# Performance work log

Measured on AMD Instinct MI355X. Metric: run time of the kernel, lower is better.

## Reference

```python
import jax, jax.numpy as jnp
import numpy as np

N, D, K = 40000, 64, 16
E = N * K
EPS = 1e-5  # torch BatchNorm1d default eps


def _bn(h, g, b):
    # BatchNorm1d in training mode: biased batch statistics over dim 0
    m = h.mean(0)
    v = h.var(0)
    return (h - m) * jax.lax.rsqrt(v + EPS) * g + b


def setup_inputs() -> dict:
    key = jax.random.key(0)
    ks = jax.random.split(key, 4)
    kp = jax.random.split(ks[3], 9)

    def w(k, shape):
        return (jax.random.normal(k, shape, dtype=jnp.float32) / np.float32(np.sqrt(shape[0])))

    src = jax.random.randint(ks[2], (E,), 0, N, dtype=jnp.int32)
    dst = jnp.repeat(jnp.arange(N, dtype=jnp.int32), K)  # kNN-style: each node has K in-edges

    return {
        "x": jax.random.normal(ks[0], (N, D), dtype=jnp.float32),
        "pos": jax.random.normal(ks[1], (N, 3), dtype=jnp.float32),
        "edge_index": jnp.stack([src, dst]),
        "W_in": w(kp[0], (D, D)),
        "g1": jnp.ones(D), "b1": jnp.zeros(D),
        "W_v": w(kp[1], (D, D)),
        "W_src": w(kp[2], (D, D)),
        "W_dst": w(kp[3], (D, D)),
        "Wp1": w(kp[4], (3, 3)), "bp1": jnp.zeros(3),
        "gp": jnp.ones(3), "bp": jnp.zeros(3),
        "Wp2": w(kp[5], (3, D)), "bp2": jnp.zeros(D),
        "ga0": jnp.ones(D), "ba0": jnp.zeros(D),
        "Wa1": w(kp[6], (D, D // 8)), "ba1": jnp.zeros(D // 8),
        "ga1": jnp.ones(D // 8), "bb1": jnp.zeros(D // 8),
        "Wa2": w(kp[7], (D // 8, D)), "ba2": jnp.zeros(D),
        "g2": jnp.ones(D), "b2": jnp.zeros(D),
        "W_out": w(kp[8], (D, D)),
        "g3": jnp.ones(D), "b3": jnp.zeros(D),
    }


def reference(x, pos, edge_index, W_in, g1, b1, W_v, W_src, W_dst,
              Wp1, bp1, gp, bp, Wp2, bp2, ga0, ba0, Wa1, ba1, ga1, bb1,
              Wa2, ba2, g2, b2, W_out, g3, b3):
    src, dst = edge_index[0], edge_index[1]  # j (source), i (dest)
    n = x.shape[0]
    x_skip = x
    h = jax.nn.relu(_bn(x @ W_in, g1, b1))

    # PointTransformerConv
    a_src = h @ W_src            # alpha_j projection [N,D]
    a_dst = h @ W_dst            # alpha_i projection [N,D]
    v = h @ W_v                  # value projection  [N,D]
    rel = pos[dst] - pos[src]    # pos_i - pos_j     [E,3]
    ph = jax.nn.relu(_bn(rel @ Wp1 + bp1, gp, bp))
    delta = ph @ Wp2 + bp2       # pos_nn output     [E,D]
    a = a_dst[dst] - a_src[src] + delta
    # attn_nn: BN -> ReLU -> (Lin+BN+ReLU) -> Lin
    a = jax.nn.relu(_bn(a, ga0, ba0))
    a = jax.nn.relu(_bn(a @ Wa1 + ba1, ga1, bb1))
    a = a @ Wa2 + ba2            # [E,D]
    # segment-wise softmax over incoming edges of each dest node
    amax = jax.lax.stop_gradient(jax.ops.segment_max(a, dst, num_segments=n))
    e = jnp.exp(a - amax[dst])
    s = jax.ops.segment_sum(e, dst, num_segments=n)
    attn = e / (s[dst] + 1e-16)  # PyG softmax adds 1e-16
    agg = jax.ops.segment_sum(attn * (v[src] + delta), dst, num_segments=n)

    h = jax.nn.relu(_bn(agg, g2, b2))
    h = _bn(h @ W_out, g3, b3)
    return jax.nn.relu(h + x_skip)
```

## Files before the change

### kernel.cpp

```cpp
#include <hip/hip_runtime.h>

#define NN 40000
#define DDIM 64
#define KE 16
#define EE 640000
#define BNEPS 1e-5f

#define WAVE_FENCE() asm volatile("" ::: "memory")

__device__ __forceinline__ void bn_coeff(const float* __restrict__ S, int C, int c,
                                         const float* __restrict__ g, const float* __restrict__ b,
                                         float inv_n, float& sc, float& sh)
{
    float m   = S[c] * inv_n;
    float var = S[C + c] * inv_n - m * m;
    float r   = rsqrtf(var + BNEPS);
    sc = g[c] * r;
    sh = b[c] - m * sc;
}

template<int TRN>
__global__ __launch_bounds__(256) void gemm64_k(
    const float* __restrict__ in,
    const float* __restrict__ W0, const float* __restrict__ W1, const float* __restrict__ W2,
    float* __restrict__ out0, float* __restrict__ out1, float* __restrict__ out2,
    const float* __restrict__ Sin, const float* __restrict__ gamma, const float* __restrict__ beta,
    float inv_n, float* __restrict__ Sout)
{
    const float* W = (blockIdx.y == 0) ? W0 : ((blockIdx.y == 1) ? W1 : W2);
    float* out     = (blockIdx.y == 0) ? out0 : ((blockIdx.y == 1) ? out1 : out2);

    __shared__ float Wl[64][64];
    __shared__ float inl[64][65];
    __shared__ float scl[64], shl[64];
    __shared__ float ssum[64], ssq[64];

    const int t = threadIdx.x;
    if (t < 64) {
        if (TRN) { float sc, sh; bn_coeff(Sin, 64, t, gamma, beta, inv_n, sc, sh); scl[t] = sc; shl[t] = sh; }
        ssum[t] = 0.f; ssq[t] = 0.f;
    }
#pragma unroll
    for (int i = 0; i < 16; i++) { int idx = t + i * 256; Wl[idx >> 6][idx & 63] = W[idx]; }
    __syncthreads();

    const int rbase = blockIdx.x * 64;
    {
        const int d = t & 63;
        float sc = 0.f, sh = 0.f;
        if (TRN) { sc = scl[d]; sh = shl[d]; }
#pragma unroll
        for (int i = 0; i < 16; i++) {
            int r = (t >> 6) + i * 4;
            float v = in[(size_t)(rbase + r) * 64 + d];
            if (TRN) v = fmaxf(fmaf(v, sc, sh), 0.f);
            inl[r][d] = v;
        }
    }
    __syncthreads();

    const int c0 = (t & 15) * 4, r0 = (t >> 4) * 4;
    float acc[4][4] = {};
#pragma unroll 16
    for (int d = 0; d < 64; d++) {
        float4 w4 = *(const float4*)&Wl[d][c0];
#pragma unroll
        for (int i = 0; i < 4; i++) {
            float h = inl[r0 + i][d];
            acc[i][0] = fmaf(h, w4.x, acc[i][0]);
            acc[i][1] = fmaf(h, w4.y, acc[i][1]);
            acc[i][2] = fmaf(h, w4.z, acc[i][2]);
            acc[i][3] = fmaf(h, w4.w, acc[i][3]);
        }
    }
#pragma unroll
    for (int i = 0; i < 4; i++) {
        float4 o; o.x = acc[i][0]; o.y = acc[i][1]; o.z = acc[i][2]; o.w = acc[i][3];
        *(float4*)&out[(size_t)(rbase + r0 + i) * 64 + c0] = o;
    }
    if (Sout) {
#pragma unroll
        for (int j = 0; j < 4; j++) {
            float s  = acc[0][j] + acc[1][j] + acc[2][j] + acc[3][j];
            float qv = acc[0][j] * acc[0][j] + acc[1][j] * acc[1][j] + acc[2][j] * acc[2][j] + acc[3][j] * acc[3][j];
            atomicAdd(&ssum[c0 + j], s);
            atomicAdd(&ssq[c0 + j], qv);
        }
        __syncthreads();
        if (t < 64) { atomicAdd(&Sout[t], ssum[t]); atomicAdd(&Sout[64 + t], ssq[t]); }
    }
}

__global__ __launch_bounds__(256) void edge_q_k(
    const float* __restrict__ pos, const int* __restrict__ src,
    const float* __restrict__ Wp1, const float* __restrict__ bp1,
    float4* __restrict__ q4, float* __restrict__ Sq)
{
    float w00 = Wp1[0], w01 = Wp1[1], w02 = Wp1[2];
    float w10 = Wp1[3], w11 = Wp1[4], w12 = Wp1[5];
    float w20 = Wp1[6], w21 = Wp1[7], w22 = Wp1[8];
    float c0 = bp1[0], c1 = bp1[1], c2 = bp1[2];
    float s0 = 0, s1 = 0, s2 = 0, p0 = 0, p1 = 0, p2 = 0;
    for (int e = blockIdx.x * blockDim.x + threadIdx.x; e < EE; e += gridDim.x * blockDim.x) {
        int sj = src[e]; int di = e >> 4;
        float r0 = pos[di * 3 + 0] - pos[sj * 3 + 0];
        float r1 = pos[di * 3 + 1] - pos[sj * 3 + 1];
        float r2 = pos[di * 3 + 2] - pos[sj * 3 + 2];
        float v0 = c0 + r0 * w00 + r1 * w10 + r2 * w20;
        float v1 = c1 + r0 * w01 + r1 * w11 + r2 * w21;
        float v2 = c2 + r0 * w02 + r1 * w12 + r2 * w22;
        float4 o; o.x = v0; o.y = v1; o.z = v2; o.w = __int_as_float(sj);
        q4[e] = o;
        s0 += v0; s1 += v1; s2 += v2;
        p0 += v0 * v0; p1 += v1 * v1; p2 += v2 * v2;
    }
#pragma unroll
    for (int o = 32; o > 0; o >>= 1) {
        s0 += __shfl_down(s0, o); s1 += __shfl_down(s1, o); s2 += __shfl_down(s2, o);
        p0 += __shfl_down(p0, o); p1 += __shfl_down(p1, o); p2 += __shfl_down(p2, o);
    }
    __shared__ float sred[4][6];
    const int w = threadIdx.x >> 6;
    if ((threadIdx.x & 63) == 0) {
        sred[w][0] = s0; sred[w][1] = s1; sred[w][2] = s2;
        sred[w][3] = p0; sred[w][4] = p1; sred[w][5] = p2;
    }
    __syncthreads();
    if (threadIdx.x < 6) {
        float v = sred[0][threadIdx.x] + sred[1][threadIdx.x] + sred[2][threadIdx.x] + sred[3][threadIdx.x];
        atomicAdd(&Sq[threadIdx.x], v);
    }
}

__global__ __launch_bounds__(256) void edge_a0_k(
    const float4* __restrict__ q4v,
    const float* __restrict__ adst, const float* __restrict__ asrc,
    const float* __restrict__ Wp2, const float* __restrict__ bp2,
    const float* __restrict__ Sq, const float* __restrict__ gp, const float* __restrict__ bp_,
    float* __restrict__ Sa0)
{
    const int lane = threadIdx.x & 63;
    const int r = lane >> 4, fq = lane & 15;
    const int wv   = blockIdx.x * (blockDim.x >> 6) + (threadIdx.x >> 6);
    const int nwv  = gridDim.x * (blockDim.x >> 6);
    const float inv_e = 1.0f / (float)EE;
    float sc30, sh30, sc31, sh31, sc32, sh32;
    bn_coeff(Sq, 3, 0, gp, bp_, inv_e, sc30, sh30);
    bn_coeff(Sq, 3, 1, gp, bp_, inv_e, sc31, sh31);
    bn_coeff(Sq, 3, 2, gp, bp_, inv_e, sc32, sh32);
    float4 w0_4 = *(const float4*)&Wp2[fq * 4];
    float4 w1_4 = *(const float4*)&Wp2[64 + fq * 4];
    float4 w2_4 = *(const float4*)&Wp2[128 + fq * 4];
    float4 bd4  = *(const float4*)&bp2[fq * 4];
    float4 s4 = {0.f,0.f,0.f,0.f}, p4 = {0.f,0.f,0.f,0.f};

    for (int i = wv; i < NN; i += nwv) {
        const int e0 = i << 4;
        float4 ad4 = *(const float4*)&adst[(size_t)i * 64 + fq * 4];
        float4 qs  = q4v[e0 + (lane & 15)];
        int sv = __float_as_int(qs.w);
        int sj[4];
#pragma unroll
        for (int p = 0; p < 4; p++) sj[p] = __shfl(sv, p * 4 + r);
        float4 av[4];
#pragma unroll
        for (int p = 0; p < 4; p++) av[p] = *(const float4*)&asrc[(size_t)sj[p] * 64 + fq * 4];
#pragma unroll
        for (int p = 0; p < 4; p++) {
            int j = p * 4 + r;
            float ph0 = fmaxf(fmaf(__shfl(qs.x, j), sc30, sh30), 0.f);
            float ph1 = fmaxf(fmaf(__shfl(qs.y, j), sc31, sh31), 0.f);
            float ph2 = fmaxf(fmaf(__shfl(qs.z, j), sc32, sh32), 0.f);
            float4 a0v;
            a0v.x = ad4.x - av[p].x + bd4.x + ph0 * w0_4.x + ph1 * w1_4.x + ph2 * w2_4.x;
            a0v.y = ad4.y - av[p].y + bd4.y + ph0 * w0_4.y + ph1 * w1_4.y + ph2 * w2_4.y;
            a0v.z = ad4.z - av[p].z + bd4.z + ph0 * w0_4.z + ph1 * w1_4.z + ph2 * w2_4.z;
            a0v.w = ad4.w - av[p].w + bd4.w + ph0 * w0_4.w + ph1 * w1_4.w + ph2 * w2_4.w;
            s4.x += a0v.x; s4.y += a0v.y; s4.z += a0v.z; s4.w += a0v.w;
            p4.x = fmaf(a0v.x, a0v.x, p4.x); p4.y = fmaf(a0v.y, a0v.y, p4.y);
            p4.z = fmaf(a0v.z, a0v.z, p4.z); p4.w = fmaf(a0v.w, a0v.w, p4.w);
        }
    }
    s4.x += __shfl_xor(s4.x, 16); s4.y += __shfl_xor(s4.y, 16);
    s4.z += __shfl_xor(s4.z, 16); s4.w += __shfl_xor(s4.w, 16);
    p4.x += __shfl_xor(p4.x, 16); p4.y += __shfl_xor(p4.y, 16);
    p4.z += __shfl_xor(p4.z, 16); p4.w += __shfl_xor(p4.w, 16);
    s4.x += __shfl_xor(s4.x, 32); s4.y += __shfl_xor(s4.y, 32);
    s4.z += __shfl_xor(s4.z, 32); s4.w += __shfl_xor(s4.w, 32);
    p4.x += __shfl_xor(p4.x, 32); p4.y += __shfl_xor(p4.y, 32);
    p4.z += __shfl_xor(p4.z, 32); p4.w += __shfl_xor(p4.w, 32);

    __shared__ float ls[64], lq[64];
    if (threadIdx.x < 64) { ls[threadIdx.x] = 0.f; lq[threadIdx.x] = 0.f; }
    __syncthreads();
    if (lane < 16) {
        atomicAdd(&ls[fq * 4 + 0], s4.x); atomicAdd(&ls[fq * 4 + 1], s4.y);
        atomicAdd(&ls[fq * 4 + 2], s4.z); atomicAdd(&ls[fq * 4 + 3], s4.w);
        atomicAdd(&lq[fq * 4 + 0], p4.x); atomicAdd(&lq[fq * 4 + 1], p4.y);
        atomicAdd(&lq[fq * 4 + 2], p4.z); atomicAdd(&lq[fq * 4 + 3], p4.w);
    }
    __syncthreads();
    if (threadIdx.x < 64) { atomicAdd(&Sa0[threadIdx.x], ls[threadIdx.x]); atomicAdd(&Sa0[64 + threadIdx.x], lq[threadIdx.x]); }
}

__global__ __launch_bounds__(256) void edge_t_k(
    const float4* __restrict__ q4v,
    const float* __restrict__ adst, const float* __restrict__ asrc,
    const float* __restrict__ Wp2, const float* __restrict__ bp2,
    const float* __restrict__ Sq, const float* __restrict__ gp, const float* __restrict__ bp_,
    const float* __restrict__ Sa0, const float* __restrict__ ga0, const float* __restrict__ ba0,
    const float* __restrict__ Wa1, const float* __restrict__ ba1,
    float* __restrict__ tout, float* __restrict__ St)
{
    __shared__ float a1l[64][68];
    __shared__ float wl[64][8];
    __shared__ float red[16];
    const int t = threadIdx.x, lane = t & 63, w = t >> 6;
    const int r = lane >> 4, fq = lane & 15;
    const float inv_e = 1.0f / (float)EE;
    float sc30, sh30, sc31, sh31, sc32, sh32;
    bn_coeff(Sq, 3, 0, gp, bp_, inv_e, sc30, sh30);
    bn_coeff(Sq, 3, 1, gp, bp_, inv_e, sc31, sh31);
    bn_coeff(Sq, 3, 2, gp, bp_, inv_e, sc32, sh32);
    float4 scA4, shA4;
    bn_coeff(Sa0, 64, fq * 4 + 0, ga0, ba0, inv_e, scA4.x, shA4.x);
    bn_coeff(Sa0, 64, fq * 4 + 1, ga0, ba0, inv_e, scA4.y, shA4.y);
    bn_coeff(Sa0, 64, fq * 4 + 2, ga0, ba0, inv_e, scA4.z, shA4.z);
    bn_coeff(Sa0, 64, fq * 4 + 3, ga0, ba0, inv_e, scA4.w, shA4.w);
    float4 w0_4 = *(const float4*)&Wp2[fq * 4];
    float4 w1_4 = *(const float4*)&Wp2[64 + fq * 4];
    float4 w2_4 = *(const float4*)&Wp2[128 + fq * 4];
    float4 bd4  = *(const float4*)&bp2[fq * 4];
    for (int i = t; i < 512; i += 256) wl[i >> 3][i & 7] = Wa1[i];
    if (t < 16) red[t] = 0.f;
    __syncthreads();

    const int eLl = lane >> 2;
    const int j0  = (lane & 3) * 2;
    float bA = ba1[j0], bB = ba1[j0 + 1];
    float ssA = 0.f, spA = 0.f, ssB = 0.f, spB = 0.f;

    for (int i = blockIdx.x * 4 + w; i < NN; i += gridDim.x * 4) {
        const int e0 = i << 4;
        {
            float4 ad4 = *(const float4*)&adst[(size_t)i * 64 + fq * 4];
            float4 qs  = q4v[e0 + (lane & 15)];
            int sv = __float_as_int(qs.w);
            int sj[4];
#pragma unroll
            for (int p = 0; p < 4; p++) sj[p] = __shfl(sv, p * 4 + r);
            float4 av[4];
#pragma unroll
            for (int p = 0; p < 4; p++) av[p] = *(const float4*)&asrc[(size_t)sj[p] * 64 + fq * 4];
#pragma unroll
            for (int p = 0; p < 4; p++) {
                int j = p * 4 + r;
                float ph0 = fmaxf(fmaf(__shfl(qs.x, j), sc30, sh30), 0.f);
                float ph1 = fmaxf(fmaf(__shfl(qs.y, j), sc31, sh31), 0.f);
                float ph2 = fmaxf(fmaf(__shfl(qs.z, j), sc32, sh32), 0.f);
                float4 a1v;
                a1v.x = ad4.x - av[p].x + bd4.x + ph0 * w0_4.x + ph1 * w1_4.x + ph2 * w2_4.x;
                a1v.y = ad4.y - av[p].y + bd4.y + ph0 * w0_4.y + ph1 * w1_4.y + ph2 * w2_4.y;
                a1v.z = ad4.z - av[p].z + bd4.z + ph0 * w0_4.z + ph1 * w1_4.z + ph2 * w2_4.z;
                a1v.w = ad4.w - av[p].w + bd4.w + ph0 * w0_4.w + ph1 * w1_4.w + ph2 * w2_4.w;
                a1v.x = fmaxf(fmaf(a1v.x, scA4.x, shA4.x), 0.f);
                a1v.y = fmaxf(fmaf(a1v.y, scA4.y, shA4.y), 0.f);
                a1v.z = fmaxf(fmaf(a1v.z, scA4.z, shA4.z), 0.f);
                a1v.w = fmaxf(fmaf(a1v.w, scA4.w, shA4.w), 0.f);
                *(float4*)&a1l[w * 16 + j][fq * 4] = a1v;
            }
        }
        WAVE_FENCE();
        {
            float acc0 = bA, acc1 = bB;
#pragma unroll 16
            for (int dd = 0; dd < 64; dd++) {
                float a = a1l[w * 16 + eLl][dd];
                acc0 = fmaf(a, wl[dd][j0], acc0);
                acc1 = fmaf(a, wl[dd][j0 + 1], acc1);
            }
            int e = e0 + eLl;
            float2 o; o.x = acc0; o.y = acc1;
            *(float2*)&tout[(size_t)e * 8 + j0] = o;
            ssA += acc0; spA += acc0 * acc0;
            ssB += acc1; spB += acc1 * acc1;
        }
        WAVE_FENCE();
    }
    __syncthreads();
    atomicAdd(&red[j0], ssA);     atomicAdd(&red[j0 + 1], ssB);
    atomicAdd(&red[8 + j0], spA); atomicAdd(&red[8 + j0 + 1], spB);
    __syncthreads();
    if (t < 16) atomicAdd(&St[t], red[t]);
}

__global__ __launch_bounds__(256) void edge_final_k(
    const float* __restrict__ tin,
    const float4* __restrict__ q4v, const float* __restrict__ vv,
    const float* __restrict__ Wp2, const float* __restrict__ bp2,
    const float* __restrict__ Sq, const float* __restrict__ gp, const float* __restrict__ bp_,
    const float* __restrict__ St, const float* __restrict__ ga1, const float* __restrict__ bb1,
    const float* __restrict__ Wa2, const float* __restrict__ ba2,
    float* __restrict__ agg, float* __restrict__ Sagg)
{
    __shared__ float att_l[4][16][68];
    __shared__ float tt_l[4][16][8];
    __shared__ float ls[64], lq[64];
    const int t = threadIdx.x, lane = t & 63, w = t >> 6;
    const int r = lane >> 4, fq = lane & 15;
    const float inv_e = 1.0f / (float)EE;
    float sc3[3], sh3[3];
#pragma unroll
    for (int k = 0; k < 3; k++) bn_coeff(Sq, 3, k, gp, bp_, inv_e, sc3[k], sh3[k]);
    float sc8[8], sh8[8];
#pragma unroll
    for (int k = 0; k < 8; k++) bn_coeff(St, 8, k, ga1, bb1, inv_e, sc8[k], sh8[k]);
    float wa[8];
#pragma unroll
    for (int k = 0; k < 8; k++) wa[k] = Wa2[k * 64 + lane];
    float bad = ba2[lane];
    float4 wp0_4 = *(const float4*)&Wp2[fq * 4];
    float4 wp1_4 = *(const float4*)&Wp2[64 + fq * 4];
    float4 wp2_4 = *(const float4*)&Wp2[128 + fq * 4];
    float4 bpd4  = *(const float4*)&bp2[fq * 4];
    float4 ssum4 = {0.f, 0.f, 0.f, 0.f}, ssq4 = {0.f, 0.f, 0.f, 0.f};

    for (int nn = 0; nn < 4; nn++) {
        const int i  = blockIdx.x * 16 + nn * 4 + w;
        const int e0 = i << 4;
        if (lane < 32) {
            float4 v = *(const float4*)&tin[(size_t)e0 * 8 + lane * 4];
            ((float4*)&tt_l[w][0][0])[lane] = v;
        }
        float4 qs = q4v[e0 + (lane & 15)];
        int sv = __float_as_int(qs.w);
        WAVE_FENCE();
        {
            float ax[16];
            float m = -3.0e38f;
#pragma unroll
            for (int j = 0; j < 16; j++) {
                float4 ta = *(const float4*)&tt_l[w][j][0];
                float4 tb = *(const float4*)&tt_l[w][j][4];
                float a = bad;
                a = fmaf(fmaxf(fmaf(ta.x, sc8[0], sh8[0]), 0.f), wa[0], a);
                a = fmaf(fmaxf(fmaf(ta.y, sc8[1], sh8[1]), 0.f), wa[1], a);
                a = fmaf(fmaxf(fmaf(ta.z, sc8[2], sh8[2]), 0.f), wa[2], a);
                a = fmaf(fmaxf(fmaf(ta.w, sc8[3], sh8[3]), 0.f), wa[3], a);
                a = fmaf(fmaxf(fmaf(tb.x, sc8[4], sh8[4]), 0.f), wa[4], a);
                a = fmaf(fmaxf(fmaf(tb.y, sc8[5], sh8[5]), 0.f), wa[5], a);
                a = fmaf(fmaxf(fmaf(tb.z, sc8[6], sh8[6]), 0.f), wa[6], a);
                a = fmaf(fmaxf(fmaf(tb.w, sc8[7], sh8[7]), 0.f), wa[7], a);
                ax[j] = a; m = fmaxf(m, a);
            }
            float s = 0.f;
#pragma unroll
            for (int j = 0; j < 16; j++) { ax[j] = __expf(ax[j] - m); s += ax[j]; }
            float inv = 1.0f / (s + 1e-16f);
#pragma unroll
            for (int j = 0; j < 16; j++) att_l[w][j][lane] = ax[j] * inv;
        }
        WAVE_FENCE();
        {
            float4 acc = {0.f, 0.f, 0.f, 0.f};
#pragma unroll
            for (int p = 0; p < 4; p++) {
                int j  = p * 4 + r;
                int sj = __shfl(sv, j);
                float4 v4  = *(const float4*)&vv[(size_t)sj * 64 + fq * 4];
                float4 at4 = *(const float4*)&att_l[w][j][fq * 4];
                float ph0 = fmaxf(fmaf(__shfl(qs.x, j), sc3[0], sh3[0]), 0.f);
                float ph1 = fmaxf(fmaf(__shfl(qs.y, j), sc3[1], sh3[1]), 0.f);
                float ph2 = fmaxf(fmaf(__shfl(qs.z, j), sc3[2], sh3[2]), 0.f);
                float4 dl4;
                dl4.x = bpd4.x + ph0 * wp0_4.x + ph1 * wp1_4.x + ph2 * wp2_4.x;
                dl4.y = bpd4.y + ph0 * wp0_4.y + ph1 * wp1_4.y + ph2 * wp2_4.y;
                dl4.z = bpd4.z + ph0 * wp0_4.z + ph1 * wp1_4.z + ph2 * wp2_4.z;
                dl4.w = bpd4.w + ph0 * wp0_4.w + ph1 * wp1_4.w + ph2 * wp2_4.w;
                acc.x = fmaf(at4.x, v4.x + dl4.x, acc.x);
                acc.y = fmaf(at4.y, v4.y + dl4.y, acc.y);
                acc.z = fmaf(at4.z, v4.z + dl4.z, acc.z);
                acc.w = fmaf(at4.w, v4.w + dl4.w, acc.w);
            }
            acc.x += __shfl_xor(acc.x, 16); acc.y += __shfl_xor(acc.y, 16);
            acc.z += __shfl_xor(acc.z, 16); acc.w += __shfl_xor(acc.w, 16);
            acc.x += __shfl_xor(acc.x, 32); acc.y += __shfl_xor(acc.y, 32);
            acc.z += __shfl_xor(acc.z, 32); acc.w += __shfl_xor(acc.w, 32);
            if (lane < 16) {
                *(float4*)&agg[(size_t)i * 64 + lane * 4] = acc;
                ssum4.x += acc.x; ssum4.y += acc.y; ssum4.z += acc.z; ssum4.w += acc.w;
                ssq4.x  += acc.x * acc.x; ssq4.y += acc.y * acc.y;
                ssq4.z  += acc.z * acc.z; ssq4.w += acc.w * acc.w;
            }
        }
        WAVE_FENCE();
    }
    if (t < 64) { ls[t] = 0.f; lq[t] = 0.f; }
    __syncthreads();
    if (lane < 16) {
        atomicAdd(&ls[fq * 4 + 0], ssum4.x); atomicAdd(&ls[fq * 4 + 1], ssum4.y);
        atomicAdd(&ls[fq * 4 + 2], ssum4.z); atomicAdd(&ls[fq * 4 + 3], ssum4.w);
        atomicAdd(&lq[fq * 4 + 0], ssq4.x);  atomicAdd(&lq[fq * 4 + 1], ssq4.y);
        atomicAdd(&lq[fq * 4 + 2], ssq4.z);  atomicAdd(&lq[fq * 4 + 3], ssq4.w);
    }
    __syncthreads();
    if (t < 64) { atomicAdd(&Sagg[t], ls[t]); atomicAdd(&Sagg[64 + t], lq[t]); }
}

__global__ __launch_bounds__(256) void final_k(
    const float* __restrict__ t2, const float* __restrict__ x,
    const float* __restrict__ St2, const float* __restrict__ g3, const float* __restrict__ b3,
    float* __restrict__ out)
{
    __shared__ float scl[64], shl[64];
    const int t = threadIdx.x;
    if (t < 64) { float sc, sh; bn_coeff(St2, 64, t, g3, b3, 1.0f / (float)NN, sc, sh); scl[t] = sc; shl[t] = sh; }
    __syncthreads();
    int idx = blockIdx.x * 256 + t;
    int c0 = (idx & 15) * 4;
    const float4 a = *(const float4*)&t2[(size_t)idx * 4];
    const float4 b = *(const float4*)&x[(size_t)idx * 4];
    float4 o;
    o.x = fmaxf(fmaf(a.x, scl[c0 + 0], shl[c0 + 0]) + b.x, 0.f);
    o.y = fmaxf(fmaf(a.y, scl[c0 + 1], shl[c0 + 1]) + b.y, 0.f);
    o.z = fmaxf(fmaf(a.z, scl[c0 + 2], shl[c0 + 2]) + b.z, 0.f);
    o.w = fmaxf(fmaf(a.w, scl[c0 + 3], shl[c0 + 3]) + b.w, 0.f);
    *(float4*)&out[(size_t)idx * 4] = o;
}

extern "C" void kernel_launch(void* const* d_in, const int* in_sizes, int n_in,
                              void* d_out, int out_size, void* d_ws, size_t ws_size,
                              hipStream_t stream)
{
    const float* x    = (const float*)d_in[0];
    const float* pos  = (const float*)d_in[1];
    const int*   src  = (const int*)d_in[2];
    const float* W_in = (const float*)d_in[3];
    const float* g1   = (const float*)d_in[4];
    const float* b1   = (const float*)d_in[5];
    const float* W_v  = (const float*)d_in[6];
    const float* W_src= (const float*)d_in[7];
    const float* W_dst= (const float*)d_in[8];
    const float* Wp1  = (const float*)d_in[9];
    const float* bp1  = (const float*)d_in[10];
    const float* gp   = (const float*)d_in[11];
    const float* bp_  = (const float*)d_in[12];
    const float* Wp2  = (const float*)d_in[13];
    const float* bp2  = (const float*)d_in[14];
    const float* ga0  = (const float*)d_in[15];
    const float* ba0  = (const float*)d_in[16];
    const float* Wa1  = (const float*)d_in[17];
    const float* ba1  = (const float*)d_in[18];
    const float* ga1  = (const float*)d_in[19];
    const float* bb1  = (const float*)d_in[20];
    const float* Wa2  = (const float*)d_in[21];
    const float* ba2  = (const float*)d_in[22];
    const float* g2   = (const float*)d_in[23];
    const float* b2   = (const float*)d_in[24];
    const float* W_out= (const float*)d_in[25];
    const float* g3   = (const float*)d_in[26];
    const float* b3   = (const float*)d_in[27];
    float* out = (float*)d_out;

    float* wsf   = (float*)d_ws;
    float* S_t1  = wsf;
    float* S_q   = wsf + 128;
    float* S_a0  = wsf + 192;
    float* S_t   = wsf + 320;
    float* S_agg = wsf + 384;
    float* S_t2  = wsf + 512;
    const size_t N64 = (size_t)NN * 64;
    float* t1   = wsf + 1024;
    float* asrc = t1 + N64;
    float* adst = asrc + N64;
    float* vv   = adst + N64;
    float* q4   = vv + N64;
    float* tt   = q4 + 4 * (size_t)EE;
    float* agg  = t1;
    float* t2   = asrc;

    hipMemsetAsync(wsf, 0, 1024 * sizeof(float), stream);

    gemm64_k<0><<<dim3(625, 1), 256, 0, stream>>>(x, W_in, W_in, W_in, t1, t1, t1,
                                                  nullptr, nullptr, nullptr, 0.f, S_t1);
    gemm64_k<1><<<dim3(625, 3), 256, 0, stream>>>(t1, W_src, W_dst, W_v, asrc, adst, vv,
                                                  S_t1, g1, b1, 1.0f / (float)NN, nullptr);
    edge_q_k<<<256, 256, 0, stream>>>(pos, src, Wp1, bp1, (float4*)q4, S_q);
    edge_a0_k<<<2048, 256, 0, stream>>>((const float4*)q4, adst, asrc, Wp2, bp2, S_q, gp, bp_, S_a0);
    edge_t_k<<<2048, 256, 0, stream>>>((const float4*)q4, adst, asrc, Wp2, bp2, S_q, gp, bp_,
                                       S_a0, ga0, ba0, Wa1, ba1, tt, S_t);
    edge_final_k<<<2500, 256, 0, stream>>>(tt, (const float4*)q4, vv, Wp2, bp2, S_q, gp, bp_,
                                           S_t, ga1, bb1, Wa2, ba2, agg, S_agg);
    gemm64_k<1><<<dim3(625, 1), 256, 0, stream>>>(agg, W_out, W_out, W_out, t2, t2, t2,
                                                  S_agg, g2, b2, 1.0f / (float)NN, S_t2);
    final_k<<<2500, 256, 0, stream>>>(t2, x, S_t2, g3, b3, out);
}
```

Measured before the change: 290.9 us.

## Merge edge position kernel into first GEMM launch and reuse input tile across three projections

The independent edge position-encoding pass is folded into the first GEMM launch as extra blocks, so the two run concurrently and one launch is removed. The three-projection GEMM now loads and normalizes each input tile once and loops over the three weight matrices, rather than using three separate y-blocks that each reload the input. This cuts launch overhead and redundant input reads and BN application, at the cost of fewer blocks and serialized weight loads within each block for the projection GEMM.

```diff
diff --git a/kernel.cpp b/kernel.cpp
--- a/kernel.cpp
+++ b/kernel.cpp
@@ -19,46 +19,182 @@
     sh = b[c] - m * sc;
 }
 
-template<int TRN>
-__global__ __launch_bounds__(256) void gemm64_k(
+__global__ __launch_bounds__(256) void gemm0q_k(
+    const float* __restrict__ in, const float* __restrict__ W,
+    float* __restrict__ out, float* __restrict__ Sout,
+    const float* __restrict__ pos, const int* __restrict__ src,
+    const float* __restrict__ Wp1, const float* __restrict__ bp1,
+    float4* __restrict__ q4, float* __restrict__ Sq)
+{
+    const int t = threadIdx.x;
+    if (blockIdx.x < 625) {
+        __shared__ float Wl[64][64];
+        __shared__ float inl[64][65];
+        __shared__ float ssum[64], ssq[64];
+        if (t < 64) { ssum[t] = 0.f; ssq[t] = 0.f; }
+#pragma unroll
+        for (int i = 0; i < 16; i++) { int idx = t + i * 256; Wl[idx >> 6][idx & 63] = W[idx]; }
+        const int rbase = blockIdx.x * 64;
+        {
+            const int d = t & 63;
+#pragma unroll
+            for (int i = 0; i < 16; i++) {
+                int r = (t >> 6) + i * 4;
+                inl[r][d] = in[(size_t)(rbase + r) * 64 + d];
+            }
+        }
+        __syncthreads();
+        const int c0 = (t & 15) * 4, r0 = (t >> 4) * 4;
+        float acc[4][4] = {};
+#pragma unroll 16
+        for (int d = 0; d < 64; d++) {
+            float4 w4 = *(const float4*)&Wl[d][c0];
+#pragma unroll
+            for (int i = 0; i < 4; i++) {
+                float h = inl[r0 + i][d];
+                acc[i][0] = fmaf(h, w4.x, acc[i][0]);
+                acc[i][1] = fmaf(h, w4.y, acc[i][1]);
+                acc[i][2] = fmaf(h, w4.z, acc[i][2]);
+                acc[i][3] = fmaf(h, w4.w, acc[i][3]);
+            }
+        }
+#pragma unroll
+        for (int i = 0; i < 4; i++) {
+            float4 o; o.x = acc[i][0]; o.y = acc[i][1]; o.z = acc[i][2]; o.w = acc[i][3];
+            *(float4*)&out[(size_t)(rbase + r0 + i) * 64 + c0] = o;
+        }
+#pragma unroll
+        for (int j = 0; j < 4; j++) {
+            float s  = acc[0][j] + acc[1][j] + acc[2][j] + acc[3][j];
+            float qv = acc[0][j] * acc[0][j] + acc[1][j] * acc[1][j] + acc[2][j] * acc[2][j] + acc[3][j] * acc[3][j];
+            atomicAdd(&ssum[c0 + j], s);
+            atomicAdd(&ssq[c0 + j], qv);
+        }
+        __syncthreads();
+        if (t < 64) { atomicAdd(&Sout[t], ssum[t]); atomicAdd(&Sout[64 + t], ssq[t]); }
+    } else {
+        __shared__ float sred[4][6];
+        const int bq = blockIdx.x - 625;
+        float w00 = Wp1[0], w01 = Wp1[1], w02 = Wp1[2];
+        float w10 = Wp1[3], w11 = Wp1[4], w12 = Wp1[5];
+        float w20 = Wp1[6], w21 = Wp1[7], w22 = Wp1[8];
+        float c0 = bp1[0], c1 = bp1[1], c2 = bp1[2];
+        float s0 = 0, s1 = 0, s2 = 0, p0 = 0, p1 = 0, p2 = 0;
+        for (int e = bq * 256 + t; e < EE; e += 160 * 256) {
+            int sj = src[e]; int di = e >> 4;
+            float r0 = pos[di * 3 + 0] - pos[sj * 3 + 0];
+            float r1 = pos[di * 3 + 1] - pos[sj * 3 + 1];
+            float r2 = pos[di * 3 + 2] - pos[sj * 3 + 2];
+            float v0 = c0 + r0 * w00 + r1 * w10 + r2 * w20;
+            float v1 = c1 + r0 * w01 + r1 * w11 + r2 * w21;
+            float v2 = c2 + r0 * w02 + r1 * w12 + r2 * w22;
+            float4 o; o.x = v0; o.y = v1; o.z = v2; o.w = __int_as_float(sj);
+            q4[e] = o;
+            s0 += v0; s1 += v1; s2 += v2;
+            p0 += v0 * v0; p1 += v1 * v1; p2 += v2 * v2;
+        }
+#pragma unroll
+        for (int o = 32; o > 0; o >>= 1) {
+            s0 += __shfl_down(s0, o); s1 += __shfl_down(s1, o); s2 += __shfl_down(s2, o);
+            p0 += __shfl_down(p0, o); p1 += __shfl_down(p1, o); p2 += __shfl_down(p2, o);
+        }
+        const int w = t >> 6;
+        if ((t & 63) == 0) {
+            sred[w][0] = s0; sred[w][1] = s1; sred[w][2] = s2;
+            sred[w][3] = p0; sred[w][4] = p1; sred[w][5] = p2;
+        }
+        __syncthreads();
+        if (t < 6) {
+            float v = sred[0][t] + sred[1][t] + sred[2][t] + sred[3][t];
+            atomicAdd(&Sq[t], v);
+        }
+    }
+}
+
+__global__ __launch_bounds__(256) void gemm3_k(
     const float* __restrict__ in,
     const float* __restrict__ W0, const float* __restrict__ W1, const float* __restrict__ W2,
     float* __restrict__ out0, float* __restrict__ out1, float* __restrict__ out2,
     const float* __restrict__ Sin, const float* __restrict__ gamma, const float* __restrict__ beta,
+    float inv_n)
+{
+    __shared__ float Wl[64][64];
+    __shared__ float inl[64][65];
+    __shared__ float scl[64], shl[64];
+    const int t = threadIdx.x;
+    if (t < 64) { float sc, sh; bn_coeff(Sin, 64, t, gamma, beta, inv_n, sc, sh); scl[t] = sc; shl[t] = sh; }
+    __syncthreads();
+    const int rbase = blockIdx.x * 64;
+    {
+        const int d = t & 63;
+        float sc = scl[d], sh = shl[d];
+#pragma unroll
+        for (int i = 0; i < 16; i++) {
+            int r = (t >> 6) + i * 4;
+            float v = in[(size_t)(rbase + r) * 64 + d];
+            inl[r][d] = fmaxf(fmaf(v, sc, sh), 0.f);
+        }
+    }
+    const int c0 = (t & 15) * 4, r0 = (t >> 4) * 4;
+#pragma unroll
+    for (int ph = 0; ph < 3; ph++) {
+        const float* W = (ph == 0) ? W0 : ((ph == 1) ? W1 : W2);
+        float* out     = (ph == 0) ? out0 : ((ph == 1) ? out1 : out2);
+        __syncthreads();
+#pragma unroll
+        for (int i = 0; i < 16; i++) { int idx = t + i * 256; Wl[idx >> 6][idx & 63] = W[idx]; }
+        __syncthreads();
+        float acc[4][4] = {};
+#pragma unroll 16
+        for (int d = 0; d < 64; d++) {
+            float4 w4 = *(const float4*)&Wl[d][c0];
+#pragma unroll
+            for (int i = 0; i < 4; i++) {
+                float h = inl[r0 + i][d];
+                acc[i][0] = fmaf(h, w4.x, acc[i][0]);
+                acc[i][1] = fmaf(h, w4.y, acc[i][1]);
+                acc[i][2] = fmaf(h, w4.z, acc[i][2]);
+                acc[i][3] = fmaf(h, w4.w, acc[i][3]);
+            }
+        }
+#pragma unroll
+        for (int i = 0; i < 4; i++) {
+            float4 o; o.x = acc[i][0]; o.y = acc[i][1]; o.z = acc[i][2]; o.w = acc[i][3];
+            *(float4*)&out[(size_t)(rbase + r0 + i) * 64 + c0] = o;
+        }
+    }
+}
+
+__global__ __launch_bounds__(256) void gemm1_k(
+    const float* __restrict__ in, const float* __restrict__ W,
+    float* __restrict__ out,
+    const float* __restrict__ Sin, const float* __restrict__ gamma, const float* __restrict__ beta,
     float inv_n, float* __restrict__ Sout)
 {
-    const float* W = (blockIdx.y == 0) ? W0 : ((blockIdx.y == 1) ? W1 : W2);
-    float* out     = (blockIdx.y == 0) ? out0 : ((blockIdx.y == 1) ? out1 : out2);
-
     __shared__ float Wl[64][64];
     __shared__ float inl[64][65];
     __shared__ float scl[64], shl[64];
     __shared__ float ssum[64], ssq[64];
-
     const int t = threadIdx.x;
     if (t < 64) {
-        if (TRN) { float sc, sh; bn_coeff(Sin, 64, t, gamma, beta, inv_n, sc, sh); scl[t] = sc; shl[t] = sh; }
+        float sc, sh; bn_coeff(Sin, 64, t, gamma, beta, inv_n, sc, sh); scl[t] = sc; shl[t] = sh;
         ssum[t] = 0.f; ssq[t] = 0.f;
     }
 #pragma unroll
     for (int i = 0; i < 16; i++) { int idx = t + i * 256; Wl[idx >> 6][idx & 63] = W[idx]; }
     __syncthreads();
-
     const int rbase = blockIdx.x * 64;
     {
         const int d = t & 63;
-        float sc = 0.f, sh = 0.f;
-        if (TRN) { sc = scl[d]; sh = shl[d]; }
+        float sc = scl[d], sh = shl[d];
 #pragma unroll
         for (int i = 0; i < 16; i++) {
             int r = (t >> 6) + i * 4;
             float v = in[(size_t)(rbase + r) * 64 + d];
-            if (TRN) v = fmaxf(fmaf(v, sc, sh), 0.f);
-            inl[r][d] = v;
-        }
-    }
-    __syncthreads();
-
+            inl[r][d] = fmaxf(fmaf(v, sc, sh), 0.f);
+        }
+    }
+    __syncthreads();
     const int c0 = (t & 15) * 4, r0 = (t >> 4) * 4;
     float acc[4][4] = {};
 #pragma unroll 16
@@ -78,58 +214,15 @@
         float4 o; o.x = acc[i][0]; o.y = acc[i][1]; o.z = acc[i][2]; o.w = acc[i][3];
         *(float4*)&out[(size_t)(rbase + r0 + i) * 64 + c0] = o;
     }
-    if (Sout) {
-#pragma unroll
-        for (int j = 0; j < 4; j++) {
-            float s  = acc[0][j] + acc[1][j] + acc[2][j] + acc[3][j];
-            float qv = acc[0][j] * acc[0][j] + acc[1][j] * acc[1][j] + acc[2][j] * acc[2][j] + acc[3][j] * acc[3][j];
-            atomicAdd(&ssum[c0 + j], s);
-            atomicAdd(&ssq[c0 + j], qv);
-        }
-        __syncthreads();
-        if (t < 64) { atomicAdd(&Sout[t], ssum[t]); atomicAdd(&Sout[64 + t], ssq[t]); }
-    }
-}
-
-__global__ __launch_bounds__(256) void edge_q_k(
-    const float* __restrict__ pos, const int* __restrict__ src,
-    const float* __restrict__ Wp1, const float* __restrict__ bp1,
-    float4* __restrict__ q4, float* __restrict__ Sq)
-{
-    float w00 = Wp1[0], w01 = Wp1[1], w02 = Wp1[2];
-    float w10 = Wp1[3], w11 = Wp1[4], w12 = Wp1[5];
-    float w20 = Wp1[6], w21 = Wp1[7], w22 = Wp1[8];
-    float c0 = bp1[0], c1 = bp1[1], c2 = bp1[2];
-    float s0 = 0, s1 = 0, s2 = 0, p0 = 0, p1 = 0, p2 = 0;
-    for (int e = blockIdx.x * blockDim.x + threadIdx.x; e < EE; e += gridDim.x * blockDim.x) {
-        int sj = src[e]; int di = e >> 4;
-        float r0 = pos[di * 3 + 0] - pos[sj * 3 + 0];
-        float r1 = pos[di * 3 + 1] - pos[sj * 3 + 1];
-        float r2 = pos[di * 3 + 2] - pos[sj * 3 + 2];
-        float v0 = c0 + r0 * w00 + r1 * w10 + r2 * w20;
-        float v1 = c1 + r0 * w01 + r1 * w11 + r2 * w21;
-        float v2 = c2 + r0 * w02 + r1 * w12 + r2 * w22;
-        float4 o; o.x = v0; o.y = v1; o.z = v2; o.w = __int_as_float(sj);
-        q4[e] = o;
-        s0 += v0; s1 += v1; s2 += v2;
-        p0 += v0 * v0; p1 += v1 * v1; p2 += v2 * v2;
-    }
-#pragma unroll
-    for (int o = 32; o > 0; o >>= 1) {
-        s0 += __shfl_down(s0, o); s1 += __shfl_down(s1, o); s2 += __shfl_down(s2, o);
-        p0 += __shfl_down(p0, o); p1 += __shfl_down(p1, o); p2 += __shfl_down(p2, o);
-    }
-    __shared__ float sred[4][6];
-    const int w = threadIdx.x >> 6;
-    if ((threadIdx.x & 63) == 0) {
-        sred[w][0] = s0; sred[w][1] = s1; sred[w][2] = s2;
-        sred[w][3] = p0; sred[w][4] = p1; sred[w][5] = p2;
-    }
-    __syncthreads();
-    if (threadIdx.x < 6) {
-        float v = sred[0][threadIdx.x] + sred[1][threadIdx.x] + sred[2][threadIdx.x] + sred[3][threadIdx.x];
-        atomicAdd(&Sq[threadIdx.x], v);
-    }
+#pragma unroll
+    for (int j = 0; j < 4; j++) {
+        float s  = acc[0][j] + acc[1][j] + acc[2][j] + acc[3][j];
+        float qv = acc[0][j] * acc[0][j] + acc[1][j] * acc[1][j] + acc[2][j] * acc[2][j] + acc[3][j] * acc[3][j];
+        atomicAdd(&ssum[c0 + j], s);
+        atomicAdd(&ssq[c0 + j], qv);
+    }
+    __syncthreads();
+    if (t < 64) { atomicAdd(&Sout[t], ssum[t]); atomicAdd(&Sout[64 + t], ssq[t]); }
 }
 
 __global__ __launch_bounds__(256) void edge_a0_k(
@@ -481,17 +574,14 @@
 
     hipMemsetAsync(wsf, 0, 1024 * sizeof(float), stream);
 
-    gemm64_k<0><<<dim3(625, 1), 256, 0, stream>>>(x, W_in, W_in, W_in, t1, t1, t1,
-                                                  nullptr, nullptr, nullptr, 0.f, S_t1);
-    gemm64_k<1><<<dim3(625, 3), 256, 0, stream>>>(t1, W_src, W_dst, W_v, asrc, adst, vv,
-                                                  S_t1, g1, b1, 1.0f / (float)NN, nullptr);
-    edge_q_k<<<256, 256, 0, stream>>>(pos, src, Wp1, bp1, (float4*)q4, S_q);
+    gemm0q_k<<<785, 256, 0, stream>>>(x, W_in, t1, S_t1, pos, src, Wp1, bp1, (float4*)q4, S_q);
+    gemm3_k<<<625, 256, 0, stream>>>(t1, W_src, W_dst, W_v, asrc, adst, vv,
+                                     S_t1, g1, b1, 1.0f / (float)NN);
     edge_a0_k<<<2048, 256, 0, stream>>>((const float4*)q4, adst, asrc, Wp2, bp2, S_q, gp, bp_, S_a0);
     edge_t_k<<<2048, 256, 0, stream>>>((const float4*)q4, adst, asrc, Wp2, bp2, S_q, gp, bp_,
                                        S_a0, ga0, ba0, Wa1, ba1, tt, S_t);
     edge_final_k<<<2500, 256, 0, stream>>>(tt, (const float4*)q4, vv, Wp2, bp2, S_q, gp, bp_,
                                            S_t, ga1, bb1, Wa2, ba2, agg, S_agg);
-    gemm64_k<1><<<dim3(625, 1), 256, 0, stream>>>(agg, W_out, W_out, W_out, t2, t2, t2,
-                                                  S_agg, g2, b2, 1.0f / (float)NN, S_t2);
+    gemm1_k<<<625, 256, 0, stream>>>(agg, W_out, t2, S_agg, g2, b2, 1.0f / (float)NN, S_t2);
     final_k<<<2500, 256, 0, stream>>>(t2, x, S_t2, g3, b3, out);
 }
```

New measurement: 286.2 us. Within noise of the previous version (-1.6%).
